# Kernel tuning notes

Measured on AMD Instinct MI355X. Metric: run time of the kernel, lower is better.

Reference implementation:

```python
import jax, jax.numpy as jnp
import numpy as np
from jax import lax


def setup_inputs() -> dict:
    key = jax.random.key(0)
    k1, k2, k3, k4 = jax.random.split(key, 4)
    B, C, H, W = 4, 1024, 64, 64
    OUT = 2048
    refer_feat = jax.random.normal(k1, (B, C, H, W), jnp.float32)
    sup_feat = jax.random.normal(k2, (B, C, H, W), jnp.float32)
    # al_conv_one: Conv2d(2048 -> 2, k=3, pad=1); small init keeps offsets in a sane range
    w_off = jax.random.normal(k3, (2, 2 * C, 3, 3), jnp.float32) * 0.01
    b_off = jnp.zeros((2,), jnp.float32)
    # defConv1: DeformConv2d(1024 -> 2048, k=1, bias=False); weight is effectively [O, C]
    w_def = jax.random.normal(k4, (OUT, C), jnp.float32) * (1.0 / np.sqrt(C))
    return {"refer_feat": refer_feat, "sup_feat": sup_feat,
            "w_off": w_off, "b_off": b_off, "w_def": w_def}


def _deform_sample(feat, dy, dx):
    """Bilinear-sample feat[b,:, h+dy, w+dx] with zero padding outside. -> [B,C,H*W]"""
    B, C, H, W = feat.shape
    py = dy + jnp.arange(H, dtype=feat.dtype)[None, :, None]   # [B,H,W]
    px = dx + jnp.arange(W, dtype=feat.dtype)[None, None, :]   # [B,H,W]
    y0 = jnp.floor(py)
    x0 = jnp.floor(px)
    wy1 = py - y0   # frac weights
    wx1 = px - x0
    y0i = y0.astype(jnp.int32)
    x0i = x0.astype(jnp.int32)
    feat_flat = feat.reshape(B, C, H * W)

    def corner(yi, xi, wgt):
        valid = (yi >= 0) & (yi < H) & (xi >= 0) & (xi < W)
        idx = (jnp.clip(yi, 0, H - 1) * W + jnp.clip(xi, 0, W - 1)).reshape(B, 1, H * W)
        g = jnp.take_along_axis(feat_flat, idx, axis=2)          # [B,C,HW]
        return g * (wgt * valid.astype(feat.dtype)).reshape(B, 1, H * W)

    return (corner(y0i, x0i, (1 - wy1) * (1 - wx1))
            + corner(y0i, x0i + 1, (1 - wy1) * wx1)
            + corner(y0i + 1, x0i, wy1 * (1 - wx1))
            + corner(y0i + 1, x0i + 1, wy1 * wx1))


def reference(refer_feat, sup_feat, w_off, b_off, w_def):
    B, C, H, W = sup_feat.shape
    concat_feat = jnp.concatenate([refer_feat, sup_feat], axis=1)      # [B,2C,H,W]
    offset = lax.conv_general_dilated(
        concat_feat, w_off, window_strides=(1, 1), padding='SAME',
        dimension_numbers=('NCHW', 'OIHW', 'NCHW')) + b_off[None, :, None, None]  # [B,2,H,W]
    # torchvision DeformConv2d offset layout for k=1: channel 0 = dy, channel 1 = dx
    sampled = _deform_sample(sup_feat, offset[:, 0], offset[:, 1])     # [B,C,HW]
    out = jnp.einsum('oc,bcl->bol', w_def, sampled)                    # 1x1 conv as GEMM
    return out.reshape(B, w_def.shape[0], H, W)
```

## Files before the change

### kernel.cpp

```cpp
#include <hip/hip_runtime.h>

#define CC   1024
#define C2   2048
#define HH   64
#define WW   64
#define HW   4096
#define MOUT 2048
#define NB   4

typedef short  short8  __attribute__((ext_vector_type(8)));
typedef float  floatx4 __attribute__((ext_vector_type(4)));

static __device__ __forceinline__ unsigned short f2bf(float f) {
  unsigned int u = __builtin_bit_cast(unsigned int, f);
  u = u + 0x7FFFu + ((u >> 16) & 1u);
  return (unsigned short)(u >> 16);
}

static __device__ __forceinline__ void glds16(const unsigned short* g, unsigned short* l) {
  __builtin_amdgcn_global_load_lds(
      (const __attribute__((address_space(1))) void*)g,
      (__attribute__((address_space(3))) void*)l, 16, 0, 0);
}

__global__ __launch_bounds__(256)
void conv_off(const float* __restrict__ refer, const float* __restrict__ sup,
              const float* __restrict__ woff, float* __restrict__ off)
{
  const int cz = blockIdx.x;
  const int ry = blockIdx.y;
  const int b  = blockIdx.z;
  const int wv = threadIdx.x >> 6;
  const int w  = threadIdx.x & 63;
  const int h0 = ry * 8 + wv * 2;

  const int cc0 = cz * 32;
  const float* basep = (cz < 32)
      ? refer + ((size_t)b * CC + cc0) * HW
      : sup   + ((size_t)b * CC + (cc0 - CC)) * HW;

  const int gy0 = h0 - 1;
  const bool top_ok = (gy0 >= 0);
  const bool bot_ok = (h0 + 2 < HH);

  float a00 = 0.f, a01 = 0.f, a10 = 0.f, a11 = 0.f;

  float rn[4];
#pragma unroll
  for (int j = 0; j < 4; j++) {
    const bool ok = (j == 0) ? top_ok : (j == 3) ? bot_ok : true;
    rn[j] = ok ? basep[(gy0 + j) * WW + w] : 0.f;
  }

  for (int ci = 0; ci < 32; ci++) {
    float rc[4];
#pragma unroll
    for (int j = 0; j < 4; j++) rc[j] = rn[j];

    if (ci < 31) {
      const float* pn = basep + (size_t)(ci + 1) * HW;
#pragma unroll
      for (int j = 0; j < 4; j++) {
        const bool ok = (j == 0) ? top_ok : (j == 3) ? bot_ok : true;
        rn[j] = ok ? pn[(gy0 + j) * WW + w] : 0.f;
      }
    }

    float lft[4], rgt[4];
#pragma unroll
    for (int j = 0; j < 4; j++) {
      const float tl = __shfl(rc[j], (w - 1) & 63, 64);
      const float tr = __shfl(rc[j], (w + 1) & 63, 64);
      lft[j] = (w == 0)  ? 0.f : tl;
      rgt[j] = (w == 63) ? 0.f : tr;
    }

    const int cc = cc0 + ci;
    const float* wp0 = woff + (size_t)cc * 9;
    const float* wp1 = woff + (size_t)(C2 + cc) * 9;
#pragma unroll
    for (int ky = 0; ky < 3; ky++) {
      const float w00 = wp0[ky * 3 + 0], w01 = wp0[ky * 3 + 1], w02 = wp0[ky * 3 + 2];
      const float w10 = wp1[ky * 3 + 0], w11 = wp1[ky * 3 + 1], w12 = wp1[ky * 3 + 2];
      a00 += lft[ky]     * w00 + rc[ky]     * w01 + rgt[ky]     * w02;
      a01 += lft[ky]     * w10 + rc[ky]     * w11 + rgt[ky]     * w12;
      a10 += lft[ky + 1] * w00 + rc[ky + 1] * w01 + rgt[ky + 1] * w02;
      a11 += lft[ky + 1] * w10 + rc[ky + 1] * w11 + rgt[ky + 1] * w12;
    }
  }

  atomicAdd(&off[((b * 2 + 0) * HH + h0) * WW + w],     a00);
  atomicAdd(&off[((b * 2 + 1) * HH + h0) * WW + w],     a01);
  atomicAdd(&off[((b * 2 + 0) * HH + h0 + 1) * WW + w], a10);
  atomicAdd(&off[((b * 2 + 1) * HH + h0 + 1) * WW + w], a11);
}

__global__ __launch_bounds__(256)
void cvt_bf16(const float* __restrict__ src, unsigned short* __restrict__ dst, int n4)
{
  const int i = blockIdx.x * 256 + threadIdx.x;
  if (i < n4) {
    const float4 f = ((const float4*)src)[i];
    ushort4 u;
    u.x = f2bf(f.x); u.y = f2bf(f.y); u.z = f2bf(f.z); u.w = f2bf(f.w);
    ((ushort4*)dst)[i] = u;
  }
}

__global__ __launch_bounds__(256)
void sample_kern(const float* __restrict__ sup, const float* __restrict__ off,
                 const float* __restrict__ boff, unsigned short* __restrict__ St)
{
  const int h   = blockIdx.x;
  const int ct  = blockIdx.y;
  const int b   = blockIdx.z;
  const int tid = threadIdx.x;

  __shared__ float swy[64], swx[64];
  __shared__ int   sy0[64], sx0[64];
  __shared__ unsigned short tile[64 * 68];

  if (tid < 64) {
    const float dy = off[((b * 2 + 0) * HH + h) * WW + tid] + boff[0];
    const float dx = off[((b * 2 + 1) * HH + h) * WW + tid] + boff[1];
    const float py = dy + (float)h;
    const float px = dx + (float)tid;
    const float y0f = floorf(py), x0f = floorf(px);
    sy0[tid] = (int)y0f;  sx0[tid] = (int)x0f;
    swy[tid] = py - y0f;  swx[tid] = px - x0f;
  }
  __syncthreads();

  const int l   = tid & 63;
  const int cs0 = tid >> 6;
  const int y0 = sy0[l], x0 = sx0[l];
  const int y1 = y0 + 1, x1 = x0 + 1;
  const float wy1 = swy[l], wx1 = swx[l];
  const float wy0 = 1.f - wy1, wx0 = 1.f - wx1;
  const float vy0 = (y0 >= 0 && y0 < HH) ? 1.f : 0.f;
  const float vy1 = (y1 >= 0 && y1 < HH) ? 1.f : 0.f;
  const float vx0 = (x0 >= 0 && x0 < WW) ? 1.f : 0.f;
  const float vx1 = (x1 >= 0 && x1 < WW) ? 1.f : 0.f;
  const int cy0 = min(max(y0, 0), HH - 1), cy1 = min(max(y1, 0), HH - 1);
  const int cx0 = min(max(x0, 0), WW - 1), cx1 = min(max(x1, 0), WW - 1);
  const int i00 = cy0 * WW + cx0, i01 = cy0 * WW + cx1;
  const int i10 = cy1 * WW + cx0, i11 = cy1 * WW + cx1;
  const float w00 = wy0 * wx0 * vy0 * vx0;
  const float w01 = wy0 * wx1 * vy0 * vx1;
  const float w10 = wy1 * wx0 * vy1 * vx0;
  const float w11 = wy1 * wx1 * vy1 * vx1;

  const int cb = ct * 64;
  for (int cs = cs0; cs < 64; cs += 4) {
    const float* sp = sup + ((size_t)b * CC + cb + cs) * HW;
    const float v = w00 * sp[i00] + w01 * sp[i01] + w10 * sp[i10] + w11 * sp[i11];
    tile[cs * 68 + l] = f2bf(v);
  }
  __syncthreads();
  const int cq  = tid & 15;
  const int ls0 = tid >> 4;
  unsigned short* stb = St + ((size_t)b * HW + h * 64) * CC;
  for (int ls = ls0; ls < 64; ls += 16) {
    ushort4 pk;
    pk.x = tile[(cq * 4 + 0) * 68 + ls];
    pk.y = tile[(cq * 4 + 1) * 68 + ls];
    pk.z = tile[(cq * 4 + 2) * 68 + ls];
    pk.w = tile[(cq * 4 + 3) * 68 + ls];
    *(ushort4*)&stb[(size_t)ls * CC + cb + cq * 4] = pk;
  }
}

#define STAGE_A(s, kk) do { \
  glds16(gA + (kk),                    &lA[s][(wave * 16) * 32]); \
  glds16(gA + (size_t)128 * CC + (kk), &lA[s][(128 + wave * 16) * 32]); \
} while (0)
#define STAGE_B(s, kk) do { \
  glds16(gB + (kk),                    &lB[s][(wave * 16) * 32]); \
  glds16(gB + (size_t)128 * CC + (kk), &lB[s][(128 + wave * 16) * 32]); \
} while (0)

__global__ __launch_bounds__(512, 2)
void gemm_bt256(const unsigned short* __restrict__ A,
                const unsigned short* __restrict__ Bt,
                float* __restrict__ C)
{
  const int bb = blockIdx.z;
  const int n0 = blockIdx.x * 256;
  const int m0 = blockIdx.y * 256;
  const unsigned short* Bb = Bt + (size_t)bb * HW * CC;
  float* Cb = C + (size_t)bb * (size_t)MOUT * HW;

  __shared__ __align__(16) unsigned short lA[3][256 * 32];
  __shared__ __align__(16) unsigned short lB[3][256 * 32];

  const int tid  = threadIdx.x;
  const int wave = tid >> 6;
  const int lane = tid & 63;
  const int wmA  = (wave >> 2) * 128;
  const int wnB  = (wave & 3) * 64;
  const int lrow = lane & 15;
  const int quad = lane >> 4;
  const int rdo  = ((quad ^ ((lrow >> 1) & 3)) << 3);

  const int srow = tid >> 2;
  const int schk = (tid & 3) ^ ((tid >> 3) & 3);
  const unsigned short* gA = A  + (size_t)(m0 + srow) * CC + schk * 8;
  const unsigned short* gB = Bb + (size_t)(n0 + srow) * CC + schk * 8;

  STAGE_A(0, 0);  STAGE_B(0, 0);
  STAGE_A(1, 32); STAGE_B(1, 32);

  floatx4 acc[8][4];
#pragma unroll
  for (int i = 0; i < 8; i++)
#pragma unroll
    for (int j = 0; j < 4; j++)
      acc[i][j] = (floatx4){0.f, 0.f, 0.f, 0.f};

  asm volatile("s_waitcnt vmcnt(4)" ::: "memory");
  __builtin_amdgcn_s_barrier();
  asm volatile("" ::: "memory");

  auto tile_step = [&](int t, int cb, int sb, bool st, int vm) {
    const int k2 = (t + 2) * 32;

    short8 af[4], bfr[4];
#pragma unroll
    for (int i = 0; i < 4; i++)
      af[i] = *(const short8*)&lA[cb][(wmA + i * 16 + lrow) * 32 + rdo];
#pragma unroll
    for (int j = 0; j < 4; j++)
      bfr[j] = *(const short8*)&lB[cb][(wnB + j * 16 + lrow) * 32 + rdo];
    if (st) STAGE_A(sb, k2);
    __builtin_amdgcn_s_barrier();
    __builtin_amdgcn_s_setprio(1);
#pragma unroll
    for (int i = 0; i < 4; i++)
#pragma unroll
      for (int j = 0; j < 4; j++)
        acc[i][j] = __builtin_amdgcn_mfma_f32_16x16x32_bf16(af[i], bfr[j], acc[i][j], 0, 0, 0);
    __builtin_amdgcn_s_setprio(0);
    __builtin_amdgcn_s_barrier();

    short8 ag[4];
#pragma unroll
    for (int i = 0; i < 4; i++)
      ag[i] = *(const short8*)&lA[cb][(wmA + 64 + i * 16 + lrow) * 32 + rdo];
    if (st) STAGE_B(sb, k2);
    __builtin_amdgcn_s_barrier();
    __builtin_amdgcn_s_setprio(1);
#pragma unroll
    for (int i = 0; i < 4; i++)
#pragma unroll
      for (int j = 0; j < 4; j++)
        acc[4 + i][j] = __builtin_amdgcn_mfma_f32_16x16x32_bf16(ag[i], bfr[j], acc[4 + i][j], 0, 0, 0);
    __builtin_amdgcn_s_setprio(0);
    if (vm == 4)      asm volatile("s_waitcnt vmcnt(4)" ::: "memory");
    else if (vm == 0) asm volatile("s_waitcnt vmcnt(0)" ::: "memory");
    __builtin_amdgcn_s_barrier();
    asm volatile("" ::: "memory");
  };

#pragma unroll 1
  for (int tt = 0; tt < 30; tt += 3) {
    tile_step(tt + 0, 0, 2, true, 4);
    tile_step(tt + 1, 1, 0, true, 4);
    tile_step(tt + 2, 2, 1, true, 4);
  }
  tile_step(30, 0, 2, false, 0);
  tile_step(31, 1, 0, false, -1);

#pragma unroll
  for (int i = 0; i < 8; i++) {
    const int mbase = m0 + wmA + i * 16 + quad * 4;
#pragma unroll
    for (int j = 0; j < 4; j++) {
      const int n = n0 + wnB + j * 16 + lrow;
      float* cp = Cb + (size_t)mbase * HW + n;
#pragma unroll
      for (int r = 0; r < 4; r++)
        cp[(size_t)r * HW] = acc[i][j][r];
    }
  }
}

extern "C" void kernel_launch(void* const* d_in, const int* in_sizes, int n_in,
                              void* d_out, int out_size, void* d_ws, size_t ws_size,
                              hipStream_t stream)
{
  const float* refer = (const float*)d_in[0];
  const float* sup   = (const float*)d_in[1];
  const float* woff  = (const float*)d_in[2];
  const float* boff  = (const float*)d_in[3];
  const float* wdef  = (const float*)d_in[4];
  float* out = (float*)d_out;

  char* ws = (char*)d_ws;
  float* off            = (float*)ws;
  unsigned short* wdefb = (unsigned short*)(ws + (512u << 10));
  unsigned short* St    = (unsigned short*)(ws + (512u << 10) + (4u << 20));

  hipMemsetAsync(off, 0, (size_t)NB * 2 * HW * sizeof(float), stream);
  conv_off<<<dim3(64, 8, NB), 256, 0, stream>>>(refer, sup, woff, off);
  cvt_bf16<<<dim3((MOUT * CC / 4 + 255) / 256), 256, 0, stream>>>(wdef, wdefb, MOUT * CC / 4);
  sample_kern<<<dim3(HH, 16, NB), 256, 0, stream>>>(sup, off, boff, St);
  gemm_bt256<<<dim3(HW / 256, MOUT / 256, NB), 512, 0, stream>>>(wdefb, St, out);
}
```

Measured before the change: 387.7 us.

## Software-pipeline LDS fragment reads across tiles with double-buffered B registers

Restructures the GEMM main loop so each tile step prefetches the next tile's low-half A and B fragments while the current tile's high-half MFMAs run. B fragments are double-buffered in registers. Both global-to-LDS stages are issued at the start of each step, which cuts the barriers per tile from three to two. This is meant to hide LDS read latency behind matrix math. The cost is higher register pressure, which risks spills or lower occupancy under launch_bounds(512,2).

New measurement: 390.9 us. About the same (+0.8%).

```diff
diff --git a/kernel.cpp b/kernel.cpp
--- a/kernel.cpp
+++ b/kernel.cpp
@@ -179,6 +179,48 @@
   glds16(gB + (size_t)128 * CC + (kk), &lB[s][(128 + wave * 16) * 32]); \
 } while (0)
 
+#define RD_LOW(NBUF, BNXT) do { \
+  _Pragma("unroll") \
+  for (int i_ = 0; i_ < 4; i_++) \
+    a[i_] = *(const short8*)&lA[NBUF][(wmA + i_ * 16 + lrow) * 32 + rdo]; \
+  _Pragma("unroll") \
+  for (int j_ = 0; j_ < 4; j_++) \
+    BNXT[j_] = *(const short8*)&lB[NBUF][(wnB + j_ * 16 + lrow) * 32 + rdo]; \
+} while (0)
+
+#define MFMA16_LOW(BCUR) do { \
+  __builtin_amdgcn_s_setprio(1); \
+  _Pragma("unroll") \
+  for (int i_ = 0; i_ < 4; i_++) \
+    _Pragma("unroll") \
+    for (int j_ = 0; j_ < 4; j_++) \
+      acc[i_][j_] = __builtin_amdgcn_mfma_f32_16x16x32_bf16(a[i_], BCUR[j_], acc[i_][j_], 0, 0, 0); \
+  __builtin_amdgcn_s_setprio(0); \
+} while (0)
+
+#define MFMA16_HIGH(BCUR) do { \
+  __builtin_amdgcn_s_setprio(1); \
+  _Pragma("unroll") \
+  for (int i_ = 0; i_ < 4; i_++) \
+    _Pragma("unroll") \
+    for (int j_ = 0; j_ < 4; j_++) \
+      acc[4 + i_][j_] = __builtin_amdgcn_mfma_f32_16x16x32_bf16(g[i_], BCUR[j_], acc[4 + i_][j_], 0, 0, 0); \
+  __builtin_amdgcn_s_setprio(0); \
+} while (0)
+
+#define TILE_STEP(T, CB, SB, NBUF, BCUR, BNXT) do { \
+  _Pragma("unroll") \
+  for (int i_ = 0; i_ < 4; i_++) \
+    g[i_] = *(const short8*)&lA[CB][(wmA + 64 + i_ * 16 + lrow) * 32 + rdo]; \
+  { const int k2_ = ((T) + 2) * 32; STAGE_A(SB, k2_); STAGE_B(SB, k2_); } \
+  MFMA16_LOW(BCUR); \
+  asm volatile("s_waitcnt vmcnt(4)" ::: "memory"); \
+  __builtin_amdgcn_s_barrier(); \
+  RD_LOW(NBUF, BNXT); \
+  MFMA16_HIGH(BCUR); \
+  __builtin_amdgcn_s_barrier(); \
+} while (0)
+
 __global__ __launch_bounds__(512, 2)
 void gemm_bt256(const unsigned short* __restrict__ A,
                 const unsigned short* __restrict__ Bt,
@@ -217,58 +259,40 @@
     for (int j = 0; j < 4; j++)
       acc[i][j] = (floatx4){0.f, 0.f, 0.f, 0.f};
 
+  short8 a[4], g[4], bX[4], bY[4];
+
   asm volatile("s_waitcnt vmcnt(4)" ::: "memory");
   __builtin_amdgcn_s_barrier();
-  asm volatile("" ::: "memory");
-
-  auto tile_step = [&](int t, int cb, int sb, bool st, int vm) {
-    const int k2 = (t + 2) * 32;
-
-    short8 af[4], bfr[4];
-#pragma unroll
-    for (int i = 0; i < 4; i++)
-      af[i] = *(const short8*)&lA[cb][(wmA + i * 16 + lrow) * 32 + rdo];
-#pragma unroll
-    for (int j = 0; j < 4; j++)
-      bfr[j] = *(const short8*)&lB[cb][(wnB + j * 16 + lrow) * 32 + rdo];
-    if (st) STAGE_A(sb, k2);
+  RD_LOW(0, bX);
+
+#pragma unroll 1
+  for (int t = 0; t < 30; t += 6) {
+    TILE_STEP(t + 0, 0, 2, 1, bX, bY);
+    TILE_STEP(t + 1, 1, 0, 2, bY, bX);
+    TILE_STEP(t + 2, 2, 1, 0, bX, bY);
+    TILE_STEP(t + 3, 0, 2, 1, bY, bX);
+    TILE_STEP(t + 4, 1, 0, 2, bX, bY);
+    TILE_STEP(t + 5, 2, 1, 0, bY, bX);
+  }
+
+  {
+#pragma unroll
+    for (int i_ = 0; i_ < 4; i_++)
+      g[i_] = *(const short8*)&lA[0][(wmA + 64 + i_ * 16 + lrow) * 32 + rdo];
+    MFMA16_LOW(bX);
+    asm volatile("s_waitcnt vmcnt(0)" ::: "memory");
     __builtin_amdgcn_s_barrier();
-    __builtin_amdgcn_s_setprio(1);
-#pragma unroll
-    for (int i = 0; i < 4; i++)
-#pragma unroll
-      for (int j = 0; j < 4; j++)
-        acc[i][j] = __builtin_amdgcn_mfma_f32_16x16x32_bf16(af[i], bfr[j], acc[i][j], 0, 0, 0);
-    __builtin_amdgcn_s_setprio(0);
+    RD_LOW(1, bY);
+    MFMA16_HIGH(bX);
     __builtin_amdgcn_s_barrier();
-
-    short8 ag[4];
-#pragma unroll
-    for (int i = 0; i < 4; i++)
-      ag[i] = *(const short8*)&lA[cb][(wmA + 64 + i * 16 + lrow) * 32 + rdo];
-    if (st) STAGE_B(sb, k2);
-    __builtin_amdgcn_s_barrier();
-    __builtin_amdgcn_s_setprio(1);
-#pragma unroll
-    for (int i = 0; i < 4; i++)
-#pragma unroll
-      for (int j = 0; j < 4; j++)
-        acc[4 + i][j] = __builtin_amdgcn_mfma_f32_16x16x32_bf16(ag[i], bfr[j], acc[4 + i][j], 0, 0, 0);
-    __builtin_amdgcn_s_setprio(0);
-    if (vm == 4)      asm volatile("s_waitcnt vmcnt(4)" ::: "memory");
-    else if (vm == 0) asm volatile("s_waitcnt vmcnt(0)" ::: "memory");
-    __builtin_amdgcn_s_barrier();
-    asm volatile("" ::: "memory");
-  };
-
-#pragma unroll 1
-  for (int tt = 0; tt < 30; tt += 3) {
-    tile_step(tt + 0, 0, 2, true, 4);
-    tile_step(tt + 1, 1, 0, true, 4);
-    tile_step(tt + 2, 2, 1, true, 4);
-  }
-  tile_step(30, 0, 2, false, 0);
-  tile_step(31, 1, 0, false, -1);
+  }
+  {
+#pragma unroll
+    for (int i_ = 0; i_ < 4; i_++)
+      g[i_] = *(const short8*)&lA[1][(wmA + 64 + i_ * 16 + lrow) * 32 + rdo];
+    MFMA16_LOW(bY);
+    MFMA16_HIGH(bY);
+  }
 
 #pragma unroll
   for (int i = 0; i < 8; i++) {
```
